# Kernel tuning notes

Measured on AMD Instinct MI355X. Metric: run time of the kernel, lower is better.

Reference implementation:

```python
import jax, jax.numpy as jnp
import numpy as np

EPS = 1e-05
SCALING = 1.0


def setup_inputs() -> dict:
    key = jax.random.key(0)
    k0, k1, k2, k3, k4, k5 = jax.random.split(key, 6)
    Nx = Ny = Nz = 160          # output grid resolution per axis
    D = 48                      # factor (Kronecker) rank per axis
    W = 3                       # width0: output channels (3D flow)
    NP = 2_000_000              # query points
    K = 8                       # interpolation taps per point (trilinear)
    x = jax.random.normal(k0, (Nx, D), dtype=jnp.float32)
    y = jax.random.normal(k1, (Ny, D), dtype=jnp.float32)
    z = jax.random.normal(k2, (Nz, D), dtype=jnp.float32)
    # matches torch init: 2/sqrt(W)*rand - 1/sqrt(W)
    weight = (2.0 / np.sqrt(W)) * jax.random.uniform(k3, (W, D, D, D), dtype=jnp.float32) - (1.0 / np.sqrt(W))
    B_idx = jax.random.randint(k4, (NP, K), 0, Nx * Ny * Nz, dtype=jnp.int32)
    B_w = jax.random.uniform(k5, (NP, K), dtype=jnp.float32)
    return {"x": x, "y": y, "z": z, "weight": weight, "B_idx": B_idx, "B_w": B_w}


def reference(x, y, z, weight, B_idx, B_w):
    # Tensor-mode (Kronecker) matmuls: (W,D0,D1,D2) -> (W,Nx,Ny,Nz)
    g = jnp.einsum('ap,wpqr->waqr', x, weight)   # contract mode-0
    g = jnp.einsum('bq,waqr->wabr', y, g)        # contract mode-1
    g = jnp.einsum('cr,wabr->wabc', z, g)        # contract mode-2
    # Total-variation regularizer (isotropic, per-voxel sqrt, channel-summed)
    base = g[:, :-1, :-1, :-1]
    tv = jnp.mean(
        jnp.sqrt(
            EPS
            + (g[:, :-1, :-1, 1:] - base) ** 2
            + (g[:, :-1, 1:, :-1] - base) ** 2
            + (g[:, 1:, :-1, :-1] - base) ** 2
        ).sum(axis=0)
    )
    reg_scaled = tv * SCALING
    # Gather-weighted interpolation: flat grid (Ncells, W), K taps per point
    flat = g.reshape(g.shape[0], -1).T            # (Nx*Ny*Nz, W)
    out = (flat[B_idx] * B_w[..., None]).sum(axis=1)  # (NP, W)
    return out, reg_scaled
```

## Files before the change

kernel.cpp:

```cpp
#include <hip/hip_runtime.h>
#include <hip/hip_fp16.h>

#define D 48
#define W 3
#define NX 160
#define NY 160
#define NZ 160
#define NPTS (NX*NY*NZ)
#define KNBR 8
#define EPSV 1e-5f
#define NTV (159*159*159)
#define NBTV 2048
#define TVROWS (159*159)
#define CPAIRS 80
#define TVSLOTS (TVROWS*CPAIRS)
#define FBLK (NBTV*3)
#define GBLK (NBTV*2)

typedef int   vint4   __attribute__((ext_vector_type(4)));
typedef float vfloat4 __attribute__((ext_vector_type(4)));

#define T1_OFF 0
#define T1_SZ (W*NX*D*D)
#define TVP_OFF (T1_OFF + T1_SZ)
#define G3_OFF (TVP_OFF + NBTV)

__device__ inline void unpack3(uint2 u, float& f0, float& f1, float& f2) {
    __half2 lo = *reinterpret_cast<__half2*>(&u.x);
    __half2 hi = *reinterpret_cast<__half2*>(&u.y);
    f0 = __low2float(lo);
    f1 = __high2float(lo);
    f2 = __low2float(hi);
}

__global__ __launch_bounds__(256) void k1(const float* __restrict__ x,
                                          const float* __restrict__ wt,
                                          float* __restrict__ t1) {
    int lane = threadIdx.x & 63;
    int wv   = threadIdx.x >> 6;
    int q    = blockIdx.x * 4 + wv;
    int a0   = blockIdx.y * 16;
    int w    = blockIdx.z;
    bool act = lane < D;

    float wreg[D];
#pragma unroll
    for (int p = 0; p < D; ++p)
        wreg[p] = act ? wt[((w*D + p)*D + q)*D + lane] : 0.f;

    for (int ai = 0; ai < 16; ++ai) {
        int a = a0 + ai;
        const float4* xp = (const float4*)(x + a*D);
        float s = 0.f;
#pragma unroll
        for (int j = 0; j < D/4; ++j) {
            float4 xv = xp[j];
            s += xv.x * wreg[4*j+0];
            s += xv.y * wreg[4*j+1];
            s += xv.z * wreg[4*j+2];
            s += xv.w * wreg[4*j+3];
        }
        if (act) t1[((w*NX + a)*D + q)*D + lane] = s;
    }
}

#define BH 20
__global__ __launch_bounds__(192) void kbcd(const float* __restrict__ y,
                                            const float* __restrict__ z,
                                            const float* __restrict__ t1,
                                            uint2* __restrict__ g3h) {
    __shared__ float t1s[W*D*D];
    __shared__ float t2s[W*BH*D];
    int tid = threadIdx.x;
    int a   = blockIdx.y;
    int b0  = blockIdx.x * BH;

    int c = tid;
    bool act = c < NZ;
    float zreg[D];
#pragma unroll
    for (int j = 0; j < D/4; ++j) {
        float4 zv = act ? ((const float4*)(z + c*D))[j] : make_float4(0,0,0,0);
        zreg[4*j+0] = zv.x; zreg[4*j+1] = zv.y; zreg[4*j+2] = zv.z; zreg[4*j+3] = zv.w;
    }

    for (int i = tid; i < W*D*D; i += 192) {
        int w = i / (D*D), rem = i - w*(D*D);
        t1s[i] = t1[(size_t)(w*NX + a)*(D*D) + rem];
    }
    __syncthreads();

    for (int i = tid; i < W*BH*(D/4); i += 192) {
        int w   = i / (BH*(D/4));
        int rem = i - w*(BH*(D/4));
        int bh  = rem / (D/4);
        int r4  = rem - bh*(D/4);
        const float4* yb  = (const float4*)(y + (b0 + bh)*D);
        const float4* t1v = (const float4*)(t1s + w*D*D) + r4;
        float4 s = make_float4(0,0,0,0);
#pragma unroll
        for (int q4 = 0; q4 < D/4; ++q4) {
            float4 yv = yb[q4];
#pragma unroll
            for (int u = 0; u < 4; ++u) {
                float yq = (u==0) ? yv.x : (u==1) ? yv.y : (u==2) ? yv.z : yv.w;
                float4 tv = t1v[(q4*4+u)*(D/4)];
                s.x += yq*tv.x; s.y += yq*tv.y; s.z += yq*tv.z; s.w += yq*tv.w;
            }
        }
        ((float4*)t2s)[i] = s;
    }
    __syncthreads();

    for (int bh = 0; bh < BH; ++bh) {
        float acc[W];
#pragma unroll
        for (int w = 0; w < W; ++w) {
            const float4* t2v = (const float4*)(t2s + (w*BH + bh)*D);
            float s = 0.f;
#pragma unroll
            for (int j = 0; j < D/4; ++j) {
                float4 t = t2v[j];
                s += t.x*zreg[4*j+0] + t.y*zreg[4*j+1] + t.z*zreg[4*j+2] + t.w*zreg[4*j+3];
            }
            acc[w] = s;
        }
        if (act) {
            __half2 lo = __halves2half2(__float2half_rn(acc[0]), __float2half_rn(acc[1]));
            __half2 hi = __halves2half2(__float2half_rn(acc[2]), __float2half_rn(0.f));
            uint2 u;
            u.x = *reinterpret_cast<unsigned*>(&lo);
            u.y = *reinterpret_cast<unsigned*>(&hi);
            g3h[(size_t)((a*NY + (b0+bh))*NZ + c)] = u;
        }
    }
}

__device__ inline float tv3(uint2 u0, uint2 uc, uint2 ub, uint2 ua) {
    float b0,b1,b2, c0,c1,c2, d0,d1,d2, e0,e1,e2;
    unpack3(u0,b0,b1,b2); unpack3(uc,c0,c1,c2);
    unpack3(ub,d0,d1,d2); unpack3(ua,e0,e1,e2);
    float x0=c0-b0, y0=d0-b0, z0=e0-b0;
    float x1=c1-b1, y1=d1-b1, z1=e1-b1;
    float x2=c2-b2, y2=d2-b2, z2=e2-b2;
    return sqrtf(EPSV + x0*x0 + y0*y0 + z0*z0)
         + sqrtf(EPSV + x1*x1 + y1*y1 + z1*z1)
         + sqrtf(EPSV + x2*x2 + y2*y2 + z2*z2);
}

__global__ __launch_bounds__(256) void ktvg(const uint2* __restrict__ g3h,
                                            float* __restrict__ partial,
                                            const int* __restrict__ bidx,
                                            const float* __restrict__ bw,
                                            float* __restrict__ out,
                                            int np) {
    int blk = blockIdx.x;
    if (blk % 3 == 2) {
        int tvb = blk / 3;
        float v = 0.f;
        for (int s = tvb * 256 + threadIdx.x; s < TVSLOTS; s += NBTV * 256) {
            int c2  = s % CPAIRS;
            int row = s / CPAIRS;
            int b   = row % 159;
            int a   = row / 159;
            int c   = 2*c2;
            size_t p = (size_t)(a*NY + b)*NZ + c;
            uint4 u0 = *(const uint4*)(g3h + p);
            uint4 ub = *(const uint4*)(g3h + p + NZ);
            uint4 ua = *(const uint4*)(g3h + p + NY*NZ);
            uint2 un = g3h[p + 2];
            uint2 u0l = make_uint2(u0.x, u0.y), u0h = make_uint2(u0.z, u0.w);
            uint2 ubl = make_uint2(ub.x, ub.y), ubh = make_uint2(ub.z, ub.w);
            uint2 ual = make_uint2(ua.x, ua.y), uah = make_uint2(ua.z, ua.w);
            v += tv3(u0l, u0h, ubl, ual);
            if (c + 1 < 159)
                v += tv3(u0h, un, ubh, uah);
        }
#pragma unroll
        for (int off = 32; off > 0; off >>= 1)
            v += __shfl_down(v, off, 64);
        __shared__ float sred[4];
        int lane = threadIdx.x & 63, wv = threadIdx.x >> 6;
        if (lane == 0) sred[wv] = v;
        __syncthreads();
        if (threadIdx.x == 0)
            partial[tvb] = sred[0] + sred[1] + sred[2] + sred[3];
        return;
    }

    int gb  = (blk / 3) * 2 + (blk % 3);
    int gid = gb * 256 + threadIdx.x;
    int half = np >> 1;
    if (gid >= half) return;
    int n1 = gid, n2 = gid + half;

    const vint4*   ip = (const vint4*)bidx;
    const vfloat4* wp = (const vfloat4*)bw;
    vint4   i0 = __builtin_nontemporal_load(ip + (size_t)n1*2);
    vint4   i1 = __builtin_nontemporal_load(ip + (size_t)n1*2 + 1);
    vint4   j0 = __builtin_nontemporal_load(ip + (size_t)n2*2);
    vint4   j1 = __builtin_nontemporal_load(ip + (size_t)n2*2 + 1);
    vfloat4 w0 = __builtin_nontemporal_load(wp + (size_t)n1*2);
    vfloat4 w1 = __builtin_nontemporal_load(wp + (size_t)n1*2 + 1);
    vfloat4 v0 = __builtin_nontemporal_load(wp + (size_t)n2*2);
    vfloat4 v1 = __builtin_nontemporal_load(wp + (size_t)n2*2 + 1);

    int   idsA[KNBR] = {i0.x, i0.y, i0.z, i0.w, i1.x, i1.y, i1.z, i1.w};
    int   idsB[KNBR] = {j0.x, j0.y, j0.z, j0.w, j1.x, j1.y, j1.z, j1.w};
    float wwsA[KNBR] = {w0.x, w0.y, w0.z, w0.w, w1.x, w1.y, w1.z, w1.w};
    float wwsB[KNBR] = {v0.x, v0.y, v0.z, v0.w, v1.x, v1.y, v1.z, v1.w};

    uint2 uA[KNBR], uB[KNBR];
#pragma unroll
    for (int k = 0; k < KNBR; ++k) uA[k] = g3h[(size_t)idsA[k]];
#pragma unroll
    for (int k = 0; k < KNBR; ++k) uB[k] = g3h[(size_t)idsB[k]];

    float a0=0.f, a1=0.f, a2=0.f, b0=0.f, b1=0.f, b2=0.f;
#pragma unroll
    for (int k = 0; k < KNBR; ++k) {
        float f0,f1,f2;
        unpack3(uA[k], f0,f1,f2);
        a0 += f0*wwsA[k]; a1 += f1*wwsA[k]; a2 += f2*wwsA[k];
    }
#pragma unroll
    for (int k = 0; k < KNBR; ++k) {
        float f0,f1,f2;
        unpack3(uB[k], f0,f1,f2);
        b0 += f0*wwsB[k]; b1 += f1*wwsB[k]; b2 += f2*wwsB[k];
    }
    float* opA = out + (size_t)n1*3;
    float* opB = out + (size_t)n2*3;
    __builtin_nontemporal_store(a0, opA+0);
    __builtin_nontemporal_store(a1, opA+1);
    __builtin_nontemporal_store(a2, opA+2);
    __builtin_nontemporal_store(b0, opB+0);
    __builtin_nontemporal_store(b1, opB+1);
    __builtin_nontemporal_store(b2, opB+2);
}

__global__ __launch_bounds__(256) void kred(const float* __restrict__ partial,
                                            float* __restrict__ outreg) {
    float v = 0.f;
    for (int i = threadIdx.x; i < NBTV; i += 256) v += partial[i];
#pragma unroll
    for (int off = 32; off > 0; off >>= 1)
        v += __shfl_down(v, off, 64);
    __shared__ float sred[4];
    int lane = threadIdx.x & 63, wv = threadIdx.x >> 6;
    if (lane == 0) sred[wv] = v;
    __syncthreads();
    if (threadIdx.x == 0)
        outreg[0] = (sred[0] + sred[1] + sred[2] + sred[3]) * (1.0f / (float)NTV);
}

extern "C" void kernel_launch(void* const* d_in, const int* in_sizes, int n_in,
                              void* d_out, int out_size, void* d_ws, size_t ws_size,
                              hipStream_t stream) {
    const float* x    = (const float*)d_in[0];
    const float* y    = (const float*)d_in[1];
    const float* z    = (const float*)d_in[2];
    const float* wt   = (const float*)d_in[3];
    const int*   bidx = (const int*)d_in[4];
    const float* bw   = (const float*)d_in[5];
    float* out = (float*)d_out;
    float* ws  = (float*)d_ws;

    float* t1  = ws + T1_OFF;
    float* tvp = ws + TVP_OFF;
    uint2* g3h = (uint2*)(ws + G3_OFF);
    int np = in_sizes[4] / KNBR;

    k1  <<<dim3(12, 10, 3), 256, 0, stream>>>(x, wt, t1);
    kbcd<<<dim3(NY/BH, NX), 192, 0, stream>>>(y, z, t1, g3h);

    ktvg<<<dim3(FBLK), 256, 0, stream>>>(g3h, tvp, bidx, bw, out, np);
    kred<<<dim3(1),    256, 0, stream>>>(tvp, out + (out_size - 1));
}
```

Measured before the change: 495.1 us.

## Register-tile kbcd mode-2 contraction and reuse shared memory for z

Rewrites the kbcd kernel so the final z contraction uses 2x4 output micro-tiles per thread (2 b rows by 4 c columns across 3 channels). Z is staged transposed in shared memory, reusing the t1 region, instead of 48 floats per thread in registers. The t1 and t2 shared layouts are padded and reordered to cut bank conflicts, and the block grows to 256 threads. The aim is more arithmetic per shared load and lower register pressure, at the cost of an extra barrier and scattered 8-byte global stores.

```diff
diff --git a/kernel.cpp b/kernel.cpp
--- a/kernel.cpp
+++ b/kernel.cpp
@@ -65,73 +65,91 @@
 }
 
 #define BH 20
-__global__ __launch_bounds__(192) void kbcd(const float* __restrict__ y,
+#define ZTPAD 196
+#define RPAD 52
+#define T1ZONE 7840
+__global__ __launch_bounds__(256) void kbcd(const float* __restrict__ y,
                                             const float* __restrict__ z,
                                             const float* __restrict__ t1,
                                             uint2* __restrict__ g3h) {
-    __shared__ float t1s[W*D*D];
-    __shared__ float t2s[W*BH*D];
+    __shared__ float smem[T1ZONE + BH*W*RPAD];
+    float* t1s = smem;
+    float* zt  = smem;
+    float* t2s = smem + T1ZONE;
     int tid = threadIdx.x;
     int a   = blockIdx.y;
     int b0  = blockIdx.x * BH;
 
-    int c = tid;
-    bool act = c < NZ;
-    float zreg[D];
-#pragma unroll
-    for (int j = 0; j < D/4; ++j) {
-        float4 zv = act ? ((const float4*)(z + c*D))[j] : make_float4(0,0,0,0);
-        zreg[4*j+0] = zv.x; zreg[4*j+1] = zv.y; zreg[4*j+2] = zv.z; zreg[4*j+3] = zv.w;
-    }
-
-    for (int i = tid; i < W*D*D; i += 192) {
+    for (int i = tid; i < W*D*D; i += 256) {
         int w = i / (D*D), rem = i - w*(D*D);
-        t1s[i] = t1[(size_t)(w*NX + a)*(D*D) + rem];
-    }
-    __syncthreads();
-
-    for (int i = tid; i < W*BH*(D/4); i += 192) {
-        int w   = i / (BH*(D/4));
-        int rem = i - w*(BH*(D/4));
-        int bh  = rem / (D/4);
-        int r4  = rem - bh*(D/4);
-        const float4* yb  = (const float4*)(y + (b0 + bh)*D);
-        const float4* t1v = (const float4*)(t1s + w*D*D) + r4;
-        float4 s = make_float4(0,0,0,0);
+        int q = rem / D,   r   = rem - q*D;
+        t1s[(q*3 + w)*RPAD + r] = t1[(size_t)(w*NX + a)*(D*D) + rem];
+    }
+    __syncthreads();
+
+    for (int i = tid; i < BH*W*(D/4); i += 256) {
+        int r4 = i % (D/4);
+        int t  = i / (D/4);
+        int w  = t % 3, bh = t / 3;
+        const vfloat4* yb = (const vfloat4*)(y + (b0 + bh)*D);
+        vfloat4 s = 0;
 #pragma unroll
         for (int q4 = 0; q4 < D/4; ++q4) {
-            float4 yv = yb[q4];
+            vfloat4 yv = yb[q4];
 #pragma unroll
             for (int u = 0; u < 4; ++u) {
-                float yq = (u==0) ? yv.x : (u==1) ? yv.y : (u==2) ? yv.z : yv.w;
-                float4 tv = t1v[(q4*4+u)*(D/4)];
-                s.x += yq*tv.x; s.y += yq*tv.y; s.z += yq*tv.z; s.w += yq*tv.w;
+                vfloat4 tv = *(const vfloat4*)(t1s + ((q4*4+u)*3 + w)*RPAD + r4*4);
+                s += yv[u] * tv;
             }
         }
-        ((float4*)t2s)[i] = s;
-    }
-    __syncthreads();
-
-    for (int bh = 0; bh < BH; ++bh) {
-        float acc[W];
-#pragma unroll
-        for (int w = 0; w < W; ++w) {
-            const float4* t2v = (const float4*)(t2s + (w*BH + bh)*D);
-            float s = 0.f;
-#pragma unroll
-            for (int j = 0; j < D/4; ++j) {
-                float4 t = t2v[j];
-                s += t.x*zreg[4*j+0] + t.y*zreg[4*j+1] + t.z*zreg[4*j+2] + t.w*zreg[4*j+3];
+        *(vfloat4*)(t2s + t*RPAD + r4*4) = s;
+    }
+    __syncthreads();
+
+    for (int i = tid; i < NZ*(D/4); i += 256) {
+        int c  = i / (D/4);
+        int j4 = i - c*(D/4);
+        vfloat4 zv = ((const vfloat4*)(z + c*D))[j4];
+        float* dst = zt + (c >> 2)*ZTPAD + (c & 3);
+#pragma unroll
+        for (int k = 0; k < 4; ++k)
+            dst[(j4*4 + k)*4] = zv[k];
+    }
+    __syncthreads();
+
+    for (int slot = tid; slot < 400; slot += 256) {
+        int g = slot % 10;
+        int h = slot / 10;
+        const float* t2b = t2s + (6*g)*RPAD;
+        const float* ztb = zt + h*ZTPAD;
+        vfloat4 acc[2][3] = {};
+#pragma unroll
+        for (int j = 0; j < D/4; ++j) {
+            vfloat4 zr0 = *(const vfloat4*)(ztb + j*16);
+            vfloat4 zr1 = *(const vfloat4*)(ztb + j*16 + 4);
+            vfloat4 zr2 = *(const vfloat4*)(ztb + j*16 + 8);
+            vfloat4 zr3 = *(const vfloat4*)(ztb + j*16 + 12);
+#pragma unroll
+            for (int u = 0; u < 6; ++u) {
+                vfloat4 T = *(const vfloat4*)(t2b + u*RPAD + j*4);
+                acc[u/3][u%3] += T[0]*zr0 + T[1]*zr1 + T[2]*zr2 + T[3]*zr3;
             }
-            acc[w] = s;
-        }
-        if (act) {
-            __half2 lo = __halves2half2(__float2half_rn(acc[0]), __float2half_rn(acc[1]));
-            __half2 hi = __halves2half2(__float2half_rn(acc[2]), __float2half_rn(0.f));
-            uint2 u;
-            u.x = *reinterpret_cast<unsigned*>(&lo);
-            u.y = *reinterpret_cast<unsigned*>(&hi);
-            g3h[(size_t)((a*NY + (b0+bh))*NZ + c)] = u;
+        }
+#pragma unroll
+        for (int bl = 0; bl < 2; ++bl) {
+            int b = b0 + 2*g + bl;
+#pragma unroll
+            for (int v = 0; v < 4; ++v) {
+                int c = 4*h + v;
+                __half2 lo = __halves2half2(__float2half_rn(acc[bl][0][v]),
+                                            __float2half_rn(acc[bl][1][v]));
+                __half2 hi = __halves2half2(__float2half_rn(acc[bl][2][v]),
+                                            __float2half_rn(0.f));
+                uint2 uu;
+                uu.x = *reinterpret_cast<unsigned*>(&lo);
+                uu.y = *reinterpret_cast<unsigned*>(&hi);
+                g3h[(size_t)(a*NY + b)*NZ + c] = uu;
+            }
         }
     }
 }
@@ -272,7 +290,7 @@
     int np = in_sizes[4] / KNBR;
 
     k1  <<<dim3(12, 10, 3), 256, 0, stream>>>(x, wt, t1);
-    kbcd<<<dim3(NY/BH, NX), 192, 0, stream>>>(y, z, t1, g3h);
+    kbcd<<<dim3(NY/BH, NX), 256, 0, stream>>>(y, z, t1, g3h);
 
     ktvg<<<dim3(FBLK), 256, 0, stream>>>(g3h, tvp, bidx, bw, out, np);
     kred<<<dim3(1),    256, 0, stream>>>(tvp, out + (out_size - 1));
```

After: 485.1 us. 1.02x faster.
